# Kernel tuning notes

Hardware: AMD Instinct MI355X
Metric: run time of the kernel (lower is better)

Reference implementation:

```python
import jax, jax.numpy as jnp
import numpy as np

E = 1024   # embed_dim
H = 16     # num_heads
D = E // H # head_dim = 64
S = 8192   # cache length
LN_EPS = 1e-6  # flax LayerNorm default


def _ln(x, scale, bias):
    m = jnp.mean(x, axis=-1, keepdims=True)
    v = jnp.mean(jnp.square(x - m), axis=-1, keepdims=True)
    return (x - m) * jax.lax.rsqrt(v + LN_EPS) * scale + bias


def setup_inputs() -> dict:
    key = jax.random.key(0)
    ks = jax.random.split(key, 16)
    w = lambda k, shape: jax.random.normal(k, shape, jnp.float32) * 0.02
    return {
        "x": jax.random.normal(ks[0], (E,), jnp.float32),
        "cache": jax.random.normal(ks[1], (2, S, H, D), jnp.float32),
        "Wv": w(ks[2], (E, E)), "bv": jnp.zeros((E,), jnp.float32),
        "Wq": w(ks[3], (E, E)), "bq": jnp.zeros((E,), jnp.float32),
        "Wk": w(ks[4], (E, E)), "bk": jnp.zeros((E,), jnp.float32),
        "Wo": w(ks[5], (E, E)), "bo": jnp.zeros((E,), jnp.float32),
        "W1": w(ks[6], (E, E)), "b1": jnp.zeros((E,), jnp.float32),
        "W2": w(ks[7], (E, E)), "b2": jnp.zeros((E,), jnp.float32),
        "ln1_s": jnp.ones((E,), jnp.float32), "ln1_b": jnp.zeros((E,), jnp.float32),
        "ln2_s": jnp.ones((E,), jnp.float32), "ln2_b": jnp.zeros((E,), jnp.float32),
        "eval_flag": 1,
    }


def reference(x, cache, Wv, bv, Wq, bq, Wk, bk, Wo, bo,
              W1, b1, W2, b2, ln1_s, ln1_b, ln2_s, ln2_b, eval_flag):
    # --- attention with shifting KV cache ---
    v_i = (x @ Wv + bv).reshape(1, H, D)
    q_i = (x @ Wq + bq).reshape(H, D)
    k_i = (x @ Wk + bk).reshape(1, H, D)
    v = jnp.concatenate((cache[0, 1:], v_i), axis=0)  # [S, H, D]
    k = jnp.concatenate((cache[1, 1:], k_i), axis=0)  # [S, H, D]
    mask = jnp.any(v != 0, axis=(1, 2))               # [S]
    attn = jnp.einsum('hd,khd->hk', q_i, k) / jnp.sqrt(jnp.float32(D))
    attn = jnp.where(mask, attn, -jnp.inf)
    attn = jax.nn.softmax(attn, axis=-1)              # [H, S]
    values = jnp.einsum('hk,khd->hd', attn, v).reshape(E)
    out_i = values @ Wo + bo
    new_cache = jnp.stack([v, k])                     # [2, S, H, D]

    # --- residual + LN + FFN (dropout deterministic => identity) ---
    h = _ln(x + out_i, ln1_s, ln1_b)
    ff = jax.nn.relu(h @ W1 + b1) @ W2 + b2
    h = _ln(h + ff, ln2_s, ln2_b)
    return (h, new_cache)
```

## Files before the change

kernel.cpp:

```cpp
#include <hip/hip_runtime.h>
#include <hip/hip_bf16.h>

#define SLEN 8192
#define EDIM 1024
#define NB   512

typedef float f4 __attribute__((ext_vector_type(4)));


__device__ inline float2 blockSum512_2(float2 v, float2* lds) {
#pragma unroll
    for (int off = 32; off; off >>= 1) {
        v.x += __shfl_xor(v.x, off);
        v.y += __shfl_xor(v.y, off);
    }
    int w = threadIdx.x >> 6, ln = threadIdx.x & 63;
    __syncthreads();
    if (ln == 0) lds[w] = v;
    __syncthreads();
    float2 s = {0.f, 0.f};
#pragma unroll
    for (int i = 0; i < 8; ++i) { s.x += lds[i].x; s.y += lds[i].y; }
    return s;
}

__device__ inline float2 blockSum1024_2(float2 v, float2* lds) {
#pragma unroll
    for (int off = 32; off; off >>= 1) {
        v.x += __shfl_xor(v.x, off);
        v.y += __shfl_xor(v.y, off);
    }
    int w = threadIdx.x >> 6, ln = threadIdx.x & 63;
    __syncthreads();
    if (ln == 0) lds[w] = v;
    __syncthreads();
    float2 s = {0.f, 0.f};
#pragma unroll
    for (int i = 0; i < 16; ++i) { s.x += lds[i].x; s.y += lds[i].y; }
    return s;
}

__global__ __launch_bounds__(256) void qkv_partial(
    const float* __restrict__ Wq, const float* __restrict__ Wk,
    const float* __restrict__ Wv, const float* __restrict__ x,
    float* __restrict__ part) {
    int cg_ = blockIdx.x;
    int m = cg_ >> 2;
    const float* W = (m == 0) ? Wq : ((m == 1) ? Wk : Wv);
    int col = (cg_ & 3) * 256 + threadIdx.x;
    int r0 = blockIdx.y * 64;
    float acc = 0.f;
#pragma unroll 16
    for (int r = 0; r < 64; ++r)
        acc = fmaf(x[r0 + r], W[(r0 + r) * EDIM + col], acc);
    part[((size_t)m * 16 + blockIdx.y) * EDIM + col] = acc;
}

__global__ __launch_bounds__(512) void attn_main(
    const float* __restrict__ cache,
    const float* __restrict__ qkvp,
    const float* __restrict__ bq, const float* __restrict__ bk,
    const float* __restrict__ bv,
    float* __restrict__ nv, float* __restrict__ nk,
    float* __restrict__ l2, float* __restrict__ acc2) {
    __shared__ float qs_l[1024];
    __shared__ float sw[8][16];
    __shared__ float sacc[8][16][64];
    float* kivi = &sacc[0][0][0];

    int tid = threadIdx.x;
    int w = tid >> 6, ld = tid & 63;
    int s0 = blockIdx.x * 16 + w * 2;

#pragma unroll
    for (int j = 0; j < 2; ++j) {
        int c = tid + 512 * j;
        float v = bq[c];
#pragma unroll
        for (int sl = 0; sl < 16; ++sl) v += qkvp[sl * EDIM + c];
        qs_l[c] = v * 0.125f;
    }
    if (blockIdx.x == NB - 1) {
#pragma unroll
        for (int j = 0; j < 2; ++j) {
            int c = tid + 512 * j;
            float vv_ = bv[c], kk_ = bk[c];
#pragma unroll
            for (int sl = 0; sl < 16; ++sl) {
                vv_ += qkvp[(32 + sl) * EDIM + c];
                kk_ += qkvp[(16 + sl) * EDIM + c];
            }
            kivi[c] = vv_;
            kivi[1024 + c] = kk_;
        }
    }
    __syncthreads();

    f4 vv[2][4], kv[2][4], q4[4];
#pragma unroll
    for (int p = 0; p < 2; ++p) {
        int s = s0 + p;
        if (s < SLEN - 1) {
            const float* vsrc = cache + (size_t)(s + 1) * EDIM;
            const float* ksrc = cache + (size_t)(SLEN + s + 1) * EDIM;
#pragma unroll
            for (int it = 0; it < 4; ++it)
                vv[p][it] = *(const f4*)(vsrc + it * 256 + ld * 4);
#pragma unroll
            for (int it = 0; it < 4; ++it)
                kv[p][it] = *(const f4*)(ksrc + it * 256 + ld * 4);
        } else {
#pragma unroll
            for (int it = 0; it < 4; ++it) {
                vv[p][it] = *(const f4*)&kivi[it * 256 + ld * 4];
                kv[p][it] = *(const f4*)&kivi[1024 + it * 256 + ld * 4];
            }
        }
    }
#pragma unroll
    for (int it = 0; it < 4; ++it)
        q4[it] = *(const f4*)&qs_l[it * 256 + ld * 4];

#pragma unroll
    for (int p = 0; p < 2; ++p) {
        int s = s0 + p;
#pragma unroll
        for (int it = 0; it < 4; ++it)
            *(f4*)(nv + (size_t)s * EDIM + it * 256 + ld * 4) = vv[p][it];
#pragma unroll
        for (int it = 0; it < 4; ++it)
            *(f4*)(nk + (size_t)s * EDIM + it * 256 + ld * 4) = kv[p][it];
    }

    float wgsum[4];
    f4 acc[4];
#pragma unroll
    for (int it = 0; it < 4; ++it) {
        wgsum[it] = 0.f;
        acc[it] = (f4){0.f, 0.f, 0.f, 0.f};
    }
#pragma unroll
    for (int p = 0; p < 2; ++p) {
        unsigned nzb = 0u;
#pragma unroll
        for (int it = 0; it < 4; ++it)
            nzb |= __float_as_uint(vv[p][it].x) | __float_as_uint(vv[p][it].y) |
                   __float_as_uint(vv[p][it].z) | __float_as_uint(vv[p][it].w);
        float sc[4];
#pragma unroll
        for (int it = 0; it < 4; ++it) {
            float d = q4[it].x * kv[p][it].x + q4[it].y * kv[p][it].y +
                      q4[it].z * kv[p][it].z + q4[it].w * kv[p][it].w;
            d += __shfl_xor(d, 1);
            d += __shfl_xor(d, 2);
            d += __shfl_xor(d, 4);
            d += __shfl_xor(d, 8);
            sc[it] = d;
        }
        bool allz = (__ballot(nzb != 0u) == 0ull);
#pragma unroll
        for (int it = 0; it < 4; ++it) {
            float wg = allz ? 0.f : __expf(sc[it]);
            wgsum[it] += wg;
            acc[it].x = fmaf(wg, vv[p][it].x, acc[it].x);
            acc[it].y = fmaf(wg, vv[p][it].y, acc[it].y);
            acc[it].z = fmaf(wg, vv[p][it].z, acc[it].z);
            acc[it].w = fmaf(wg, vv[p][it].w, acc[it].w);
        }
    }
    if ((ld & 15) == 0) {
#pragma unroll
        for (int it = 0; it < 4; ++it) sw[w][it * 4 + (ld >> 4)] = wgsum[it];
    }
    __syncthreads();

#pragma unroll
    for (int it = 0; it < 4; ++it) {
        int h = it * 4 + (ld >> 4);
        *(f4*)&sacc[w][h][(ld & 15) * 4] = acc[it];
    }
    __syncthreads();

#pragma unroll
    for (int j = 0; j < 2; ++j) {
        int h = 2 * w + j;
        float a = 0.f;
#pragma unroll
        for (int ww = 0; ww < 8; ++ww) a += sacc[ww][h][ld];
        acc2[(size_t)blockIdx.x * 1024 + h * 64 + ld] = a;
        if (ld == 0) {
            float l = 0.f;
#pragma unroll
            for (int ww = 0; ww < 8; ++ww) l += sw[ww][h];
            l2[blockIdx.x * 16 + h] = l;
        }
    }
}

__global__ __launch_bounds__(256) void attn_red(
    const float* __restrict__ l2, const float* __restrict__ acc2,
    float* __restrict__ l3g, float* __restrict__ acc3) {
    __shared__ float sA[4][64];
    __shared__ float sLl[4][16];
    int cx = blockIdx.x, g = blockIdx.y;
    int t = threadIdx.x, w = t >> 6, ld = t & 63;
    int p0 = g * 64 + w * 16;
    float a = 0.f;
#pragma unroll
    for (int i = 0; i < 16; ++i)
        a += acc2[(size_t)(p0 + i) * 1024 + cx * 64 + ld];
    sA[w][ld] = a;
    if (cx == 0 && ld < 16) {
        float l = 0.f;
#pragma unroll
        for (int i = 0; i < 16; ++i) l += l2[(p0 + i) * 16 + ld];
        sLl[w][ld] = l;
    }
    __syncthreads();
    if (w == 0) {
        acc3[(size_t)g * 1024 + cx * 64 + ld] =
            sA[0][ld] + sA[1][ld] + sA[2][ld] + sA[3][ld];
        if (cx == 0 && ld < 16)
            l3g[g * 16 + ld] = sLl[0][ld] + sLl[1][ld] + sLl[2][ld] + sLl[3][ld];
    }
}

__global__ __launch_bounds__(512) void gemv_wo(
    const float* __restrict__ Wo,
    const float* __restrict__ l3g, const float* __restrict__ acc3,
    float* __restrict__ part) {
    __shared__ float vals[64];
    __shared__ float sred[2][256];
    int by = blockIdx.y;
    int t = threadIdx.x;
    if (t < 64) {
        float a = 0.f, L = 0.f;
#pragma unroll
        for (int g = 0; g < 8; ++g) {
            a += acc3[(size_t)g * 1024 + by * 64 + t];
            L += l3g[g * 16 + by];
        }
        vals[t] = a / L;
    }
    __syncthreads();
    int half = t >> 8, tc = t & 255;
    int col = blockIdx.x * 256 + tc;
    float acc = 0.f;
#pragma unroll 16
    for (int r = 0; r < 32; ++r)
        acc = fmaf(vals[half * 32 + r],
                   Wo[(size_t)(by * 64 + half * 32 + r) * EDIM + col], acc);
    sred[half][tc] = acc;
    __syncthreads();
    if (t < 256)
        part[(size_t)by * EDIM + blockIdx.x * 256 + t] = sred[0][t] + sred[1][t];
}

__global__ __launch_bounds__(512) void gemv_w1(
    const float* __restrict__ W1, const float* __restrict__ gp1,
    const float* __restrict__ bo, const float* __restrict__ x,
    const float* __restrict__ ln1s, const float* __restrict__ ln1b,
    float* __restrict__ h1, float* __restrict__ part) {
    __shared__ float r_l[1024];
    __shared__ float2 red[8];
    __shared__ float vals[64];
    __shared__ float sred[2][256];
    int t = threadIdx.x;
    float2 ss = {0.f, 0.f};
#pragma unroll
    for (int j = 0; j < 2; ++j) {
        int i = t + 512 * j;
        float v = x[i] + bo[i];
#pragma unroll
        for (int sl = 0; sl < 16; ++sl) v += gp1[(size_t)sl * EDIM + i];
        r_l[i] = v;
        ss.x += v; ss.y += v * v;
    }
    float2 s = blockSum512_2(ss, red);
    float mean = s.x * (1.f / 1024.f);
    float var = s.y * (1.f / 1024.f) - mean * mean;
    float rstd = rsqrtf(var + 1e-6f);
    int by = blockIdx.y;
    if (t < 64) {
        int row = by * 64 + t;
        float hv = (r_l[row] - mean) * rstd * ln1s[row] + ln1b[row];
        vals[t] = hv;
        if (blockIdx.x == 0) h1[row] = hv;
    }
    __syncthreads();
    int half = t >> 8, tc = t & 255;
    int col = blockIdx.x * 256 + tc;
    float acc = 0.f;
#pragma unroll 16
    for (int r = 0; r < 32; ++r)
        acc = fmaf(vals[half * 32 + r],
                   W1[(size_t)(by * 64 + half * 32 + r) * EDIM + col], acc);
    sred[half][tc] = acc;
    __syncthreads();
    if (t < 256)
        part[(size_t)by * EDIM + blockIdx.x * 256 + t] = sred[0][t] + sred[1][t];
}

__global__ __launch_bounds__(512) void gemv_w2(
    const float* __restrict__ W2, const float* __restrict__ gp2,
    const float* __restrict__ b1, float* __restrict__ part) {
    __shared__ float vals[64];
    __shared__ float sred[2][256];
    int by = blockIdx.y;
    int t = threadIdx.x;
    if (t < 64) {
        int r = by * 64 + t;
        float v = b1[r];
#pragma unroll
        for (int sl = 0; sl < 16; ++sl) v += gp2[(size_t)sl * EDIM + r];
        vals[t] = fmaxf(v, 0.f);
    }
    __syncthreads();
    int half = t >> 8, tc = t & 255;
    int col = blockIdx.x * 256 + tc;
    float acc = 0.f;
#pragma unroll 16
    for (int r = 0; r < 32; ++r)
        acc = fmaf(vals[half * 32 + r],
                   W2[(size_t)(by * 64 + half * 32 + r) * EDIM + col], acc);
    sred[half][tc] = acc;
    __syncthreads();
    if (t < 256)
        part[(size_t)by * EDIM + blockIdx.x * 256 + t] = sred[0][t] + sred[1][t];
}

__global__ __launch_bounds__(1024) void combine_ln(
    const float* __restrict__ part, const float* __restrict__ bias,
    const float* __restrict__ resid, const float* __restrict__ g,
    const float* __restrict__ b, float* __restrict__ out) {
    __shared__ float2 lds[16];
    int t = threadIdx.x;
    float v = bias[t];
#pragma unroll
    for (int sl = 0; sl < 16; ++sl) v += part[(size_t)sl * EDIM + t];
    float r = resid[t] + v;
    float2 s = blockSum1024_2((float2){r, r * r}, lds);
    float mean = s.x * (1.f / 1024.f);
    float var = s.y * (1.f / 1024.f) - mean * mean;
    out[t] = (r - mean) * rsqrtf(var + 1e-6f) * g[t] + b[t];
}

extern "C" void kernel_launch(void* const* d_in, const int* in_sizes, int n_in,
                              void* d_out, int out_size, void* d_ws, size_t ws_size,
                              hipStream_t stream) {
    const float* x     = (const float*)d_in[0];
    const float* cache = (const float*)d_in[1];
    const float* Wv    = (const float*)d_in[2];
    const float* bv    = (const float*)d_in[3];
    const float* Wq    = (const float*)d_in[4];
    const float* bq    = (const float*)d_in[5];
    const float* Wk    = (const float*)d_in[6];
    const float* bk    = (const float*)d_in[7];
    const float* Wo    = (const float*)d_in[8];
    const float* bo    = (const float*)d_in[9];
    const float* W1    = (const float*)d_in[10];
    const float* b1    = (const float*)d_in[11];
    const float* W2    = (const float*)d_in[12];
    const float* b2    = (const float*)d_in[13];
    const float* ln1s  = (const float*)d_in[14];
    const float* ln1b  = (const float*)d_in[15];
    const float* ln2s  = (const float*)d_in[16];
    const float* ln2b  = (const float*)d_in[17];

    float* out = (float*)d_out;
    float* nv = out + 1024;
    float* nk = out + 1024 + (size_t)SLEN * EDIM;

    float* w    = (float*)d_ws;
    float* qkvp = w;
    float* l2   = qkvp + 48 * 1024;
    float* acc2 = l2 + (size_t)NB * 16;
    float* l3g  = acc2 + (size_t)NB * 1024;
    float* acc3 = l3g + 128;
    float* gp1  = acc3 + 8 * 1024;
    float* h1   = gp1 + 16 * 1024;
    float* gp2  = h1 + 1024;
    float* gp3  = gp2 + 16 * 1024;

    qkv_partial<<<dim3(12, 16), 256, 0, stream>>>(Wq, Wk, Wv, x, qkvp);
    attn_main<<<NB, 512, 0, stream>>>(cache, qkvp, bq, bk, bv, nv, nk, l2, acc2);
    attn_red<<<dim3(16, 8), 256, 0, stream>>>(l2, acc2, l3g, acc3);
    gemv_wo<<<dim3(4, 16), 512, 0, stream>>>(Wo, l3g, acc3, gp1);
    gemv_w1<<<dim3(4, 16), 512, 0, stream>>>(W1, gp1, bo, x, ln1s, ln1b, h1, gp2);
    gemv_w2<<<dim3(4, 16), 512, 0, stream>>>(W2, gp2, b1, gp3);
    combine_ln<<<1, 1024, 0, stream>>>(gp3, b2, h1, ln2s, ln2b, out);
}
```

Measured before the change: 50.42 us.

## Split attention into separate K-score/copy and V-copy blocks plus a weighted-V kernel

The fused attention kernel is split in two. The first kernel uses twice as many blocks, with half copying V and computing per-row nonzero flags and half copying K and computing per-head scores. A second kernel then re-reads the freshly written V rows along with the scores and flags to do the exp-weighted accumulation. This aims for more parallelism per block, at the cost of an extra launch and a second full read of the 32 MB V cache plus score traffic.

```diff
diff --git a/kernel.cpp b/kernel.cpp
--- a/kernel.cpp
+++ b/kernel.cpp
@@ -3,7 +3,7 @@
 
 #define SLEN 8192
 #define EDIM 1024
-#define NB   512
+#define NB2  512
 
 typedef float f4 __attribute__((ext_vector_type(4)));
 
@@ -56,82 +56,119 @@
     part[((size_t)m * 16 + blockIdx.y) * EDIM + col] = acc;
 }
 
-__global__ __launch_bounds__(512) void attn_main(
+__global__ __launch_bounds__(512) void attn_copy(
     const float* __restrict__ cache,
     const float* __restrict__ qkvp,
     const float* __restrict__ bq, const float* __restrict__ bk,
     const float* __restrict__ bv,
     float* __restrict__ nv, float* __restrict__ nk,
+    float* __restrict__ flag, float* __restrict__ score) {
+    __shared__ float qs_l[1024];
+    __shared__ float aux[1024];
+    int b = blockIdx.x, tid = threadIdx.x;
+    int w = tid >> 6, ld = tid & 63;
+    int c = b >> 1;
+    bool isK = (b & 1) != 0;
+    int s0 = c * 16 + w * 2;
+
+    if (isK) {
+#pragma unroll
+        for (int j = 0; j < 2; ++j) {
+            int i = tid + 512 * j;
+            float v = bq[i];
+#pragma unroll
+            for (int sl = 0; sl < 16; ++sl) v += qkvp[sl * EDIM + i];
+            qs_l[i] = v * 0.125f;
+        }
+        if (b == 1023) {
+#pragma unroll
+            for (int j = 0; j < 2; ++j) {
+                int i = tid + 512 * j;
+                float v = bk[i];
+#pragma unroll
+                for (int sl = 0; sl < 16; ++sl) v += qkvp[(16 + sl) * EDIM + i];
+                aux[i] = v;
+            }
+        }
+    } else if (b == 1022) {
+#pragma unroll
+        for (int j = 0; j < 2; ++j) {
+            int i = tid + 512 * j;
+            float v = bv[i];
+#pragma unroll
+            for (int sl = 0; sl < 16; ++sl) v += qkvp[(32 + sl) * EDIM + i];
+            aux[i] = v;
+        }
+    }
+    __syncthreads();
+
+    if (!isK) {
+        f4 vv[2][4];
+#pragma unroll
+        for (int p = 0; p < 2; ++p) {
+            int s = s0 + p;
+            const float* src = (s < SLEN - 1) ? cache + (size_t)(s + 1) * EDIM
+                                              : aux;
+#pragma unroll
+            for (int it = 0; it < 4; ++it)
+                vv[p][it] = *(const f4*)(src + it * 256 + ld * 4);
+        }
+#pragma unroll
+        for (int p = 0; p < 2; ++p) {
+            int s = s0 + p;
+            unsigned nzb = 0u;
+#pragma unroll
+            for (int it = 0; it < 4; ++it) {
+                *(f4*)(nv + (size_t)s * EDIM + it * 256 + ld * 4) = vv[p][it];
+                nzb |= __float_as_uint(vv[p][it].x) | __float_as_uint(vv[p][it].y) |
+                       __float_as_uint(vv[p][it].z) | __float_as_uint(vv[p][it].w);
+            }
+            bool anynz = (__ballot(nzb != 0u) != 0ull);
+            if (ld == 0) flag[s] = anynz ? 1.f : 0.f;
+        }
+    } else {
+        f4 q4[4];
+#pragma unroll
+        for (int it = 0; it < 4; ++it)
+            q4[it] = *(const f4*)&qs_l[it * 256 + ld * 4];
+        f4 kv[2][4];
+#pragma unroll
+        for (int p = 0; p < 2; ++p) {
+            int s = s0 + p;
+            const float* src = (s < SLEN - 1) ? cache + (size_t)(SLEN + s + 1) * EDIM
+                                              : aux;
+#pragma unroll
+            for (int it = 0; it < 4; ++it)
+                kv[p][it] = *(const f4*)(src + it * 256 + ld * 4);
+        }
+#pragma unroll
+        for (int p = 0; p < 2; ++p) {
+            int s = s0 + p;
+#pragma unroll
+            for (int it = 0; it < 4; ++it) {
+                *(f4*)(nk + (size_t)s * EDIM + it * 256 + ld * 4) = kv[p][it];
+                float d = q4[it].x * kv[p][it].x + q4[it].y * kv[p][it].y +
+                          q4[it].z * kv[p][it].z + q4[it].w * kv[p][it].w;
+                d += __shfl_xor(d, 1);
+                d += __shfl_xor(d, 2);
+                d += __shfl_xor(d, 4);
+                d += __shfl_xor(d, 8);
+                if ((ld & 15) == 0) score[s * 16 + it * 4 + (ld >> 4)] = d;
+            }
+        }
+    }
+}
+
+__global__ __launch_bounds__(512) void attn_wv(
+    const float* __restrict__ nv, const float* __restrict__ flag,
+    const float* __restrict__ score,
     float* __restrict__ l2, float* __restrict__ acc2) {
-    __shared__ float qs_l[1024];
     __shared__ float sw[8][16];
     __shared__ float sacc[8][16][64];
-    float* kivi = &sacc[0][0][0];
-
     int tid = threadIdx.x;
     int w = tid >> 6, ld = tid & 63;
     int s0 = blockIdx.x * 16 + w * 2;
 
-#pragma unroll
-    for (int j = 0; j < 2; ++j) {
-        int c = tid + 512 * j;
-        float v = bq[c];
-#pragma unroll
-        for (int sl = 0; sl < 16; ++sl) v += qkvp[sl * EDIM + c];
-        qs_l[c] = v * 0.125f;
-    }
-    if (blockIdx.x == NB - 1) {
-#pragma unroll
-        for (int j = 0; j < 2; ++j) {
-            int c = tid + 512 * j;
-            float vv_ = bv[c], kk_ = bk[c];
-#pragma unroll
-            for (int sl = 0; sl < 16; ++sl) {
-                vv_ += qkvp[(32 + sl) * EDIM + c];
-                kk_ += qkvp[(16 + sl) * EDIM + c];
-            }
-            kivi[c] = vv_;
-            kivi[1024 + c] = kk_;
-        }
-    }
-    __syncthreads();
-
-    f4 vv[2][4], kv[2][4], q4[4];
-#pragma unroll
-    for (int p = 0; p < 2; ++p) {
-        int s = s0 + p;
-        if (s < SLEN - 1) {
-            const float* vsrc = cache + (size_t)(s + 1) * EDIM;
-            const float* ksrc = cache + (size_t)(SLEN + s + 1) * EDIM;
-#pragma unroll
-            for (int it = 0; it < 4; ++it)
-                vv[p][it] = *(const f4*)(vsrc + it * 256 + ld * 4);
-#pragma unroll
-            for (int it = 0; it < 4; ++it)
-                kv[p][it] = *(const f4*)(ksrc + it * 256 + ld * 4);
-        } else {
-#pragma unroll
-            for (int it = 0; it < 4; ++it) {
-                vv[p][it] = *(const f4*)&kivi[it * 256 + ld * 4];
-                kv[p][it] = *(const f4*)&kivi[1024 + it * 256 + ld * 4];
-            }
-        }
-    }
-#pragma unroll
-    for (int it = 0; it < 4; ++it)
-        q4[it] = *(const f4*)&qs_l[it * 256 + ld * 4];
-
-#pragma unroll
-    for (int p = 0; p < 2; ++p) {
-        int s = s0 + p;
-#pragma unroll
-        for (int it = 0; it < 4; ++it)
-            *(f4*)(nv + (size_t)s * EDIM + it * 256 + ld * 4) = vv[p][it];
-#pragma unroll
-        for (int it = 0; it < 4; ++it)
-            *(f4*)(nk + (size_t)s * EDIM + it * 256 + ld * 4) = kv[p][it];
-    }
-
     float wgsum[4];
     f4 acc[4];
 #pragma unroll
@@ -141,39 +178,27 @@
     }
 #pragma unroll
     for (int p = 0; p < 2; ++p) {
-        unsigned nzb = 0u;
+        int s = s0 + p;
+        f4 vv[4];
 #pragma unroll
         for (int it = 0; it < 4; ++it)
-            nzb |= __float_as_uint(vv[p][it].x) | __float_as_uint(vv[p][it].y) |
-                   __float_as_uint(vv[p][it].z) | __float_as_uint(vv[p][it].w);
-        float sc[4];
+            vv[it] = *(const f4*)(nv + (size_t)s * EDIM + it * 256 + ld * 4);
+        float fl = flag[s];
 #pragma unroll
         for (int it = 0; it < 4; ++it) {
-            float d = q4[it].x * kv[p][it].x + q4[it].y * kv[p][it].y +
-                      q4[it].z * kv[p][it].z + q4[it].w * kv[p][it].w;
-            d += __shfl_xor(d, 1);
-            d += __shfl_xor(d, 2);
-            d += __shfl_xor(d, 4);
-            d += __shfl_xor(d, 8);
-            sc[it] = d;
-        }
-        bool allz = (__ballot(nzb != 0u) == 0ull);
-#pragma unroll
-        for (int it = 0; it < 4; ++it) {
-            float wg = allz ? 0.f : __expf(sc[it]);
+            int h = it * 4 + (ld >> 4);
+            float wg = (fl != 0.f) ? __expf(score[s * 16 + h]) : 0.f;
             wgsum[it] += wg;
-            acc[it].x = fmaf(wg, vv[p][it].x, acc[it].x);
-            acc[it].y = fmaf(wg, vv[p][it].y, acc[it].y);
-            acc[it].z = fmaf(wg, vv[p][it].z, acc[it].z);
-            acc[it].w = fmaf(wg, vv[p][it].w, acc[it].w);
+            acc[it].x = fmaf(wg, vv[it].x, acc[it].x);
+            acc[it].y = fmaf(wg, vv[it].y, acc[it].y);
+            acc[it].z = fmaf(wg, vv[it].z, acc[it].z);
+            acc[it].w = fmaf(wg, vv[it].w, acc[it].w);
         }
     }
     if ((ld & 15) == 0) {
 #pragma unroll
         for (int it = 0; it < 4; ++it) sw[w][it * 4 + (ld >> 4)] = wgsum[it];
     }
-    __syncthreads();
-
 #pragma unroll
     for (int it = 0; it < 4; ++it) {
         int h = it * 4 + (ld >> 4);
@@ -371,19 +396,22 @@
     float* nv = out + 1024;
     float* nk = out + 1024 + (size_t)SLEN * EDIM;
 
-    float* w    = (float*)d_ws;
-    float* qkvp = w;
-    float* l2   = qkvp + 48 * 1024;
-    float* acc2 = l2 + (size_t)NB * 16;
-    float* l3g  = acc2 + (size_t)NB * 1024;
-    float* acc3 = l3g + 128;
-    float* gp1  = acc3 + 8 * 1024;
-    float* h1   = gp1 + 16 * 1024;
-    float* gp2  = h1 + 1024;
-    float* gp3  = gp2 + 16 * 1024;
+    float* w     = (float*)d_ws;
+    float* qkvp  = w;
+    float* flag  = qkvp + 48 * 1024;
+    float* score = flag + SLEN;
+    float* l2    = score + (size_t)SLEN * 16;
+    float* acc2  = l2 + (size_t)NB2 * 16;
+    float* l3g   = acc2 + (size_t)NB2 * 1024;
+    float* acc3  = l3g + 128;
+    float* gp1   = acc3 + 8 * 1024;
+    float* h1    = gp1 + 16 * 1024;
+    float* gp2   = h1 + 1024;
+    float* gp3   = gp2 + 16 * 1024;
 
     qkv_partial<<<dim3(12, 16), 256, 0, stream>>>(Wq, Wk, Wv, x, qkvp);
-    attn_main<<<NB, 512, 0, stream>>>(cache, qkvp, bq, bk, bv, nv, nk, l2, acc2);
+    attn_copy<<<1024, 512, 0, stream>>>(cache, qkvp, bq, bk, bv, nv, nk, flag, score);
+    attn_wv<<<NB2, 512, 0, stream>>>(nv, flag, score, l2, acc2);
     attn_red<<<dim3(16, 8), 256, 0, stream>>>(l2, acc2, l3g, acc3);
     gemv_wo<<<dim3(4, 16), 512, 0, stream>>>(Wo, l3g, acc3, gp1);
     gemv_w1<<<dim3(4, 16), 512, 0, stream>>>(W1, gp1, bo, x, ln1s, ln1b, h1, gp2);
```

Result: slower. 56.67 us (+12.4%).

## Shift KV cache with a device memcpy and read attention inputs from output

Applied to the files above, without the earlier changes.

The cache shift moves out of the attention kernel into a single device-to-device memcpy from cache+EDIM into the new-cache output. The memcpy covers V rows 1..S-1, the old K row 0 in the V/K boundary slot, and K rows 1..S-1. The attention kernel then reads K and V from the shifted output and writes the new last rows, overwriting the stale K row 0 in the last V slot. This likely aims to use the driver copy path for the bulk move, but the cache data now makes two passes through memory (copy, then reload) instead of one fused load and store, adding traffic and an extra serial dependency.

```diff
diff --git a/kernel.cpp b/kernel.cpp
--- a/kernel.cpp
+++ b/kernel.cpp
@@ -3,7 +3,7 @@
 
 #define SLEN 8192
 #define EDIM 1024
-#define NB   512
+#define NBC  512
 
 typedef float f4 __attribute__((ext_vector_type(4)));
 
@@ -56,8 +56,7 @@
     part[((size_t)m * 16 + blockIdx.y) * EDIM + col] = acc;
 }
 
-__global__ __launch_bounds__(512) void attn_main(
-    const float* __restrict__ cache,
+__global__ __launch_bounds__(512) void attn_comp(
     const float* __restrict__ qkvp,
     const float* __restrict__ bq, const float* __restrict__ bk,
     const float* __restrict__ bv,
@@ -66,32 +65,33 @@
     __shared__ float qs_l[1024];
     __shared__ float sw[8][16];
     __shared__ float sacc[8][16][64];
-    float* kivi = &sacc[0][0][0];
-
+    float* aux = &sacc[0][0][0];
     int tid = threadIdx.x;
     int w = tid >> 6, ld = tid & 63;
     int s0 = blockIdx.x * 16 + w * 2;
 
 #pragma unroll
     for (int j = 0; j < 2; ++j) {
-        int c = tid + 512 * j;
-        float v = bq[c];
-#pragma unroll
-        for (int sl = 0; sl < 16; ++sl) v += qkvp[sl * EDIM + c];
-        qs_l[c] = v * 0.125f;
-    }
-    if (blockIdx.x == NB - 1) {
+        int i = tid + 512 * j;
+        float v = bq[i];
+#pragma unroll
+        for (int sl = 0; sl < 16; ++sl) v += qkvp[sl * EDIM + i];
+        qs_l[i] = v * 0.125f;
+    }
+    if (blockIdx.x == NBC - 1) {
 #pragma unroll
         for (int j = 0; j < 2; ++j) {
-            int c = tid + 512 * j;
-            float vv_ = bv[c], kk_ = bk[c];
+            int i = tid + 512 * j;
+            float vv_ = bv[i], kk_ = bk[i];
 #pragma unroll
             for (int sl = 0; sl < 16; ++sl) {
-                vv_ += qkvp[(32 + sl) * EDIM + c];
-                kk_ += qkvp[(16 + sl) * EDIM + c];
+                vv_ += qkvp[(32 + sl) * EDIM + i];
+                kk_ += qkvp[(16 + sl) * EDIM + i];
             }
-            kivi[c] = vv_;
-            kivi[1024 + c] = kk_;
+            aux[i] = vv_;
+            aux[1024 + i] = kk_;
+            nv[(size_t)(SLEN - 1) * EDIM + i] = vv_;
+            nk[(size_t)(SLEN - 1) * EDIM + i] = kk_;
         }
     }
     __syncthreads();
@@ -101,36 +101,23 @@
     for (int p = 0; p < 2; ++p) {
         int s = s0 + p;
         if (s < SLEN - 1) {
-            const float* vsrc = cache + (size_t)(s + 1) * EDIM;
-            const float* ksrc = cache + (size_t)(SLEN + s + 1) * EDIM;
 #pragma unroll
             for (int it = 0; it < 4; ++it)
-                vv[p][it] = *(const f4*)(vsrc + it * 256 + ld * 4);
+                vv[p][it] = *(const f4*)(nv + (size_t)s * EDIM + it * 256 + ld * 4);
 #pragma unroll
             for (int it = 0; it < 4; ++it)
-                kv[p][it] = *(const f4*)(ksrc + it * 256 + ld * 4);
+                kv[p][it] = *(const f4*)(nk + (size_t)s * EDIM + it * 256 + ld * 4);
         } else {
 #pragma unroll
             for (int it = 0; it < 4; ++it) {
-                vv[p][it] = *(const f4*)&kivi[it * 256 + ld * 4];
-                kv[p][it] = *(const f4*)&kivi[1024 + it * 256 + ld * 4];
+                vv[p][it] = *(const f4*)&aux[it * 256 + ld * 4];
+                kv[p][it] = *(const f4*)&aux[1024 + it * 256 + ld * 4];
             }
         }
     }
 #pragma unroll
     for (int it = 0; it < 4; ++it)
         q4[it] = *(const f4*)&qs_l[it * 256 + ld * 4];
-
-#pragma unroll
-    for (int p = 0; p < 2; ++p) {
-        int s = s0 + p;
-#pragma unroll
-        for (int it = 0; it < 4; ++it)
-            *(f4*)(nv + (size_t)s * EDIM + it * 256 + ld * 4) = vv[p][it];
-#pragma unroll
-        for (int it = 0; it < 4; ++it)
-            *(f4*)(nk + (size_t)s * EDIM + it * 256 + ld * 4) = kv[p][it];
-    }
 
     float wgsum[4];
     f4 acc[4];
@@ -374,16 +361,20 @@
     float* w    = (float*)d_ws;
     float* qkvp = w;
     float* l2   = qkvp + 48 * 1024;
-    float* acc2 = l2 + (size_t)NB * 16;
-    float* l3g  = acc2 + (size_t)NB * 1024;
+    float* acc2 = l2 + (size_t)NBC * 16;
+    float* l3g  = acc2 + (size_t)NBC * 1024;
     float* acc3 = l3g + 128;
     float* gp1  = acc3 + 8 * 1024;
     float* h1   = gp1 + 16 * 1024;
     float* gp2  = h1 + 1024;
     float* gp3  = gp2 + 16 * 1024;
 
+    hipMemcpyAsync(nv, cache + EDIM,
+                   (size_t)(2 * SLEN - 1) * EDIM * sizeof(float),
+                   hipMemcpyDeviceToDevice, stream);
+
     qkv_partial<<<dim3(12, 16), 256, 0, stream>>>(Wq, Wk, Wv, x, qkvp);
-    attn_main<<<NB, 512, 0, stream>>>(cache, qkvp, bq, bk, bv, nv, nk, l2, acc2);
+    attn_comp<<<NBC, 512, 0, stream>>>(qkvp, bq, bk, bv, nv, nk, l2, acc2);
     attn_red<<<dim3(16, 8), 256, 0, stream>>>(l2, acc2, l3g, acc3);
     gemv_wo<<<dim3(4, 16), 512, 0, stream>>>(Wo, l3g, acc3, gp1);
     gemv_w1<<<dim3(4, 16), 512, 0, stream>>>(W1, gp1, bo, x, ln1s, ln1b, h1, gp2);
```

Result: slower. 60.93 us (+20.9%).
